# Optimization experiments

Hardware: AMD Instinct MI355X
Metric: run time of the kernel (lower is better)

The kernel has to match this reference:

```python
import jax, jax.numpy as jnp
import numpy as np

B = 8          # graphs (FOVs)
NPG = 16384    # clusters per graph
N = B * NPG
K = 6          # knn k=5+1, loop=True
E = N * K
C0PG = 2048    # superclusters_0 per graph
C0 = B * C0PG
C1PG = 256     # superclusters_1 per graph
C1 = B * C1PG
L = 10         # 4 cluster-level + 3 SC0 + 3 SC1 PointTransformerConv layers
D = 64


def setup_inputs() -> dict:
    key = jax.random.key(0)
    ks = jax.random.split(key, 20)
    s = 0.05  # weight scale for stable attention logits
    x = jax.random.normal(ks[0], (N, D), jnp.float32)
    pos_c = jax.random.uniform(ks[1], (N, 2), jnp.float32)
    dst_c = jnp.repeat(jnp.arange(N, dtype=jnp.int32), K)
    src_c = jax.random.randint(ks[2], (E,), 0, N, jnp.int32)
    src_c = src_c.at[::K].set(jnp.arange(N, dtype=jnp.int32))  # self-loops
    batch = (jnp.arange(N, dtype=jnp.int32) // NPG)
    sc_id0 = (jnp.arange(N, dtype=jnp.int32) % C0PG)   # every SC0 id present per graph
    pos_sc0 = jax.random.uniform(ks[3], (C0, 2), jnp.float32)
    sc_id1 = (jnp.arange(C0, dtype=jnp.int32) % C1PG)
    pos_sc1 = jax.random.uniform(ks[4], (C1, 2), jnp.float32)
    return dict(
        x=x, pos_c=pos_c, src_c=src_c, dst_c=dst_c, batch=batch,
        sc_id0=sc_id0, pos_sc0=pos_sc0, sc_id1=sc_id1, pos_sc1=pos_sc1,
        Wlin=jax.random.normal(ks[5], (L, D, D)) * s,
        Wsrc=jax.random.normal(ks[6], (L, D, D)) * s,
        Wdst=jax.random.normal(ks[7], (L, D, D)) * s,
        pW1=jax.random.normal(ks[8], (L, 2, D)) * s,
        pB1=jnp.zeros((L, D), jnp.float32),
        pW2=jax.random.normal(ks[9], (L, D, D)) * s,
        pB2=jnp.zeros((L, D), jnp.float32),
        aW1=jax.random.normal(ks[10], (L, D, D)) * s,
        aB1=jnp.zeros((L, D), jnp.float32),
        aW2=jax.random.normal(ks[11], (L, D, D)) * s,
        aB2=jnp.zeros((L, D), jnp.float32),
        head_w=jax.random.normal(ks[12], (D, 2)) * s,
        head_b=jnp.zeros((2,), jnp.float32),
    )


def mlp2(x, W1, b1, W2, b2):
    # PyG MLP(plain_last=False): Linear->ReLU twice (eval mode, BN at init = identity)
    h = jax.nn.relu(x @ W1 + b1)
    return jax.nn.relu(h @ W2 + b2)


def ptconv(h, pos, src, dst, n, p, l):
    # PointTransformerConv: delta = pos_nn(pos_i - pos_j);
    # alpha = softmax_i(attn_nn(lin_dst(x)_i - lin_src(x)_j + delta));
    # out_i = max_j alpha * (lin(x)_j + delta)
    xv = h @ p['Wlin'][l]
    a_src = h @ p['Wsrc'][l]
    a_dst = h @ p['Wdst'][l]
    delta = mlp2(pos[dst] - pos[src], p['pW1'][l], p['pB1'][l], p['pW2'][l], p['pB2'][l])
    a = mlp2(a_dst[dst] - a_src[src] + delta, p['aW1'][l], p['aB1'][l], p['aW2'][l], p['aB2'][l])
    m = jax.ops.segment_max(a, dst, num_segments=n)
    e = jnp.exp(a - m[dst])
    ssum = jax.ops.segment_sum(e, dst, num_segments=n)
    alpha = e / ssum[dst]
    return jax.ops.segment_max(alpha * (xv[src] + delta), dst, num_segments=n)


def gen_cluster(ids, batch, nb):
    mx = jax.ops.segment_max(ids, batch, num_segments=nb)
    off = jnp.cumsum(jnp.concatenate([jnp.zeros((1,), ids.dtype), mx + 1]))
    return ids + off[batch].astype(ids.dtype)


def knn_edges(pos, b, npg, k):
    # knn_graph(k, loop=True) per graph: src=neighbor, dst=center
    p = pos.reshape(b, npg, 2)
    sq = jnp.sum(p * p, axis=-1)
    d2 = sq[:, :, None] + sq[:, None, :] - 2.0 * jnp.einsum('bnd,bmd->bnm', p, p)
    idx = jax.lax.top_k(-d2, k)[1]  # [b, npg, k], includes self (d=0)
    src = (idx + (jnp.arange(b) * npg)[:, None, None]).reshape(-1).astype(jnp.int32)
    dst = jnp.repeat(jnp.arange(b * npg, dtype=jnp.int32), k)
    return src, dst


def reference(x, pos_c, src_c, dst_c, batch, sc_id0, pos_sc0, sc_id1, pos_sc1,
              Wlin, Wsrc, Wdst, pW1, pB1, pW2, pB2, aW1, aB1, aW2, aB2,
              head_w, head_b):
    p = dict(Wlin=Wlin, Wsrc=Wsrc, Wdst=Wdst, pW1=pW1, pB1=pB1, pW2=pW2, pB2=pB2,
             aW1=aW1, aB1=aB1, aW2=aW2, aB2=aB2)
    h = x
    for l in range(4):  # cluster_encoder_0..3 on clusters graph
        h = ptconv(h, pos_c, src_c, dst_c, N, p, l)
    # pool clusters -> superclusters_0
    cl0 = gen_cluster(sc_id0, batch, B)
    h0 = jax.ops.segment_max(h, cl0, num_segments=C0)
    batch0 = jax.ops.segment_max(batch, cl0, num_segments=C0)
    src0, dst0 = knn_edges(pos_sc0, B, C0PG, K)
    for l in range(4, 7):
        h0 = ptconv(h0, pos_sc0, src0, dst0, C0, p, l)
    # pool SC0 -> superclusters_1
    cl1 = gen_cluster(sc_id1, batch0, B)
    h1 = jax.ops.segment_max(h0, cl1, num_segments=C1)
    batch1 = jax.ops.segment_max(batch0, cl1, num_segments=C1)
    src1, dst1 = knn_edges(pos_sc1, B, C1PG, K)
    for l in range(7, 10):
        h1 = ptconv(h1, pos_sc1, src1, dst1, C1, p, l)
    g = jax.ops.segment_max(h1, batch1, num_segments=B)  # global_max_pool
    return g @ head_w + head_b
```

## Files before the change

kernel.cpp:

```cpp
#include <hip/hip_runtime.h>
#include <cstdint>

namespace {
constexpr int BG   = 8;
constexpr int NPG  = 16384;
constexpr int NN   = BG * NPG;
constexpr int KK   = 6;
constexpr int C0PG = 2048;
constexpr int C0N  = BG * C0PG;
constexpr int C1PG = 256;
constexpr int C1N  = BG * C1PG;
constexpr int D    = 64;
constexpr int SEG0 = C0PG / 256;
constexpr int VS   = 198;
constexpr int NMS  = 132;
}

__device__ __forceinline__ unsigned f2u_ord(float v) {
  unsigned u = __float_as_uint(v);
  return (u & 0x80000000u) ? ~u : (u | 0x80000000u);
}

__global__ void k_init_u32(unsigned* __restrict__ p, unsigned v, int n) {
  int i = blockIdx.x * blockDim.x + threadIdx.x;
  if (i < n) p[i] = v;
}

__global__ void k_seg_max_i32(const int* __restrict__ vals, const int* __restrict__ seg,
                              int* __restrict__ out, int n) {
  int i = blockIdx.x * blockDim.x + threadIdx.x;
  if (i < n) atomicMax(&out[seg[i]], vals[i]);
}

template <int NB>
__global__ __launch_bounds__(256) void k_seg_max_small(
    const int* __restrict__ vals, const int* __restrict__ seg,
    int* __restrict__ out, int n) {
  __shared__ int lmx[NB];
  int t = threadIdx.x;
  if (t < NB) lmx[t] = (int)0x80000000;
  __syncthreads();
  for (int i = blockIdx.x * 256 + t; i < n; i += gridDim.x * 256)
    atomicMax(&lmx[seg[i]], vals[i]);
  __syncthreads();
  if (t < NB) atomicMax(&out[t], lmx[t]);
}

__global__ void k_cumsum_off(const int* __restrict__ mx, int* __restrict__ off, int nb) {
  if (threadIdx.x == 0 && blockIdx.x == 0) {
    int a = 0; off[0] = 0;
    for (int b = 0; b < nb; ++b) { a += mx[b] + 1; off[b + 1] = a; }
  }
}

__global__ void k_gen_cl(const int* __restrict__ ids, const int* __restrict__ bt,
                         const int* __restrict__ off, int* __restrict__ cl, int n) {
  int i = blockIdx.x * blockDim.x + threadIdx.x;
  if (i < n) cl[i] = ids[i] + off[bt[i]];
}

__global__ void k_pool_f32(const float* __restrict__ h, const int* __restrict__ cl,
                           unsigned* __restrict__ outu, int total) {
  int i = blockIdx.x * blockDim.x + threadIdx.x;
  if (i < total) atomicMax(&outu[(size_t)cl[i >> 6] * D + (i & 63)], f2u_ord(h[i]));
}

__global__ void k_decode_f32(unsigned* __restrict__ p, int n) {
  int i = blockIdx.x * blockDim.x + threadIdx.x;
  if (i < n) { unsigned u = p[i]; p[i] = (u & 0x80000000u) ? (u ^ 0x80000000u) : ~u; }
}

__global__ __launch_bounds__(256) void k_knn(const float* __restrict__ pos, int npg,
                                             int* __restrict__ srcOut) {
  #pragma clang fp contract(off)
  __shared__ float px[2048], py[2048], sq[2048];
  int t = threadIdx.x;
  int nglob = blockIdx.x * 256 + t;
  int graph = nglob / npg;
  int base = graph * npg;
  for (int i = t; i < npg; i += 256) {
    float xx = pos[2 * (base + i)];
    float yy = pos[2 * (base + i) + 1];
    px[i] = xx; py[i] = yy;
    float a = xx * xx; float b = yy * yy;
    sq[i] = a + b;
  }
  __syncthreads();
  int i = nglob - base;
  float xi = px[i], yi = py[i], sqi = sq[i];
  float bd[KK]; int bi[KK];
  #pragma unroll
  for (int q = 0; q < KK; ++q) { bd[q] = 3.4e38f; bi[q] = 0; }
  for (int j = 0; j < npg; ++j) {
    float t1 = xi * px[j];
    float t2 = yi * py[j];
    float dot = t1 + t2;
    float d2 = (sqi + sq[j]) - 2.0f * dot;
    if (d2 < bd[KK - 1]) {
      bd[KK - 1] = d2; bi[KK - 1] = j;
      #pragma unroll
      for (int q = KK - 1; q > 0; --q) {
        if (bd[q] < bd[q - 1]) {
          float td = bd[q]; bd[q] = bd[q - 1]; bd[q - 1] = td;
          int ti = bi[q]; bi[q] = bi[q - 1]; bi[q - 1] = ti;
        }
      }
    }
  }
  #pragma unroll
  for (int q = 0; q < KK; ++q) srcOut[(size_t)nglob * KK + q] = base + bi[q];
}

__global__ __launch_bounds__(256) void k_knn_part(const float* __restrict__ pos, int npg,
                                                  int nseg,
                                                  float* __restrict__ outD,
                                                  int* __restrict__ outI) {
  #pragma clang fp contract(off)
  __shared__ float cx[256], cy[256], cs[256];
  int t = threadIdx.x;
  int qt = blockIdx.x / nseg;
  int s  = blockIdx.x % nseg;
  int qlo = qt * 256;
  int graph = qlo / npg;
  int base = graph * npg;
  int cbase = base + s * 256;
  {
    float xx = pos[2 * (cbase + t)];
    float yy = pos[2 * (cbase + t) + 1];
    cx[t] = xx; cy[t] = yy;
    float a = xx * xx; float b = yy * yy;
    cs[t] = a + b;
  }
  __syncthreads();
  int q = qlo + t;
  float xi = pos[2 * q], yi = pos[2 * q + 1];
  float qa = xi * xi; float qb = yi * yi;
  float sqi = qa + qb;
  float bd[KK]; int bi[KK];
  #pragma unroll
  for (int u = 0; u < KK; ++u) { bd[u] = 3.4e38f; bi[u] = 0; }
  for (int j = 0; j < 256; ++j) {
    float t1 = xi * cx[j];
    float t2 = yi * cy[j];
    float dot = t1 + t2;
    float d2 = (sqi + cs[j]) - 2.0f * dot;
    if (d2 < bd[KK - 1]) {
      bd[KK - 1] = d2; bi[KK - 1] = cbase + j;
      #pragma unroll
      for (int u = KK - 1; u > 0; --u) {
        if (bd[u] < bd[u - 1]) {
          float td = bd[u]; bd[u] = bd[u - 1]; bd[u - 1] = td;
          int ti = bi[u]; bi[u] = bi[u - 1]; bi[u - 1] = ti;
        }
      }
    }
  }
  size_t ob = (size_t)q * (nseg * KK) + (size_t)s * KK;
  #pragma unroll
  for (int u = 0; u < KK; ++u) { outD[ob + u] = bd[u]; outI[ob + u] = bi[u]; }
}

__global__ void k_knn_merge(const float* __restrict__ inD, const int* __restrict__ inI,
                            int nseg, int* __restrict__ srcOut, int nq) {
  int q = blockIdx.x * blockDim.x + threadIdx.x;
  if (q >= nq) return;
  float bd[KK]; int bi[KK];
  #pragma unroll
  for (int u = 0; u < KK; ++u) { bd[u] = 3.4e38f; bi[u] = 0x7fffffff; }
  size_t ib = (size_t)q * (nseg * KK);
  for (int e = 0; e < nseg * KK; ++e) {
    float d = inD[ib + e]; int ix = inI[ib + e];
    bool lt = (d < bd[KK - 1]) || (d == bd[KK - 1] && ix < bi[KK - 1]);
    if (lt) {
      bd[KK - 1] = d; bi[KK - 1] = ix;
      #pragma unroll
      for (int u = KK - 1; u > 0; --u) {
        bool sw = (bd[u] < bd[u - 1]) || (bd[u] == bd[u - 1] && bi[u] < bi[u - 1]);
        if (sw) {
          float td = bd[u]; bd[u] = bd[u - 1]; bd[u - 1] = td;
          int ti = bi[u]; bi[u] = bi[u - 1]; bi[u - 1] = ti;
        }
      }
    }
  }
  #pragma unroll
  for (int u = 0; u < KK; ++u) srcOut[(size_t)q * KK + u] = bi[u];
}

__global__ void __launch_bounds__(256)
__attribute__((amdgpu_waves_per_eu(4, 4)))
k_node_mm(const float* __restrict__ hin,
    const float* __restrict__ Wl, const float* __restrict__ Ws, const float* __restrict__ Wd,
    float* __restrict__ xv, float* __restrict__ as_, float* __restrict__ ad_) {
  __shared__ float wbuf[2048];
  __shared__ float vbuf[32 * NMS];
  int t = threadIdx.x;
  size_t nb = (size_t)blockIdx.x * 128;
  int ng = t >> 3, cb = t & 7, c0 = cb * 8;
  const float* Wm[3] = {Wl, Ws, Wd};
  float* Om[3] = {xv, as_, ad_};
  const float4* h4 = (const float4*)hin;
  float4 wreg0 = ((const float4*)Wl)[t];
  float4 wreg1 = ((const float4*)Wl)[256 + t];
  float acc[3][32];
  #pragma unroll
  for (int m = 0; m < 3; ++m)
    #pragma unroll
    for (int i = 0; i < 32; ++i) acc[m][i] = 0.0f;
  #pragma unroll
  for (int kh = 0; kh < 2; ++kh) {
    #pragma unroll
    for (int r = 0; r < 4; ++r) {
      int flat = r * 256 + t;
      int n = flat >> 3, kq = flat & 7;
      float4 hv = h4[(nb + n) * 16 + kh * 8 + kq];
      vbuf[(kq * 4 + 0) * NMS + n] = hv.x;
      vbuf[(kq * 4 + 1) * NMS + n] = hv.y;
      vbuf[(kq * 4 + 2) * NMS + n] = hv.z;
      vbuf[(kq * 4 + 3) * NMS + n] = hv.w;
    }
    #pragma unroll
    for (int m = 0; m < 3; ++m) {
      {
        float4* wb = (float4*)wbuf;
        wb[t] = wreg0;
        wb[256 + t] = wreg1;
      }
      if (!(kh == 1 && m == 2)) {
        const float* nW = (m < 2) ? Wm[m + 1] : Wm[0];
        int nkh = (m < 2) ? kh : kh + 1;
        const float4* nxt = (const float4*)nW + nkh * 512;
        wreg0 = nxt[t];
        wreg1 = nxt[256 + t];
      }
      __syncthreads();
      #pragma clang loop unroll_count(2)
      for (int kk = 0; kk < 32; ++kk) {
        float4 v4 = *(const float4*)&vbuf[kk * NMS + 4 * ng];
        float4 w0 = *(const float4*)&wbuf[kk * 64 + c0];
        float4 w1 = *(const float4*)&wbuf[kk * 64 + c0 + 4];
        float vv[4] = {v4.x, v4.y, v4.z, v4.w};
        float wv[8] = {w0.x, w0.y, w0.z, w0.w, w1.x, w1.y, w1.z, w1.w};
        #pragma unroll
        for (int ni = 0; ni < 4; ++ni)
          #pragma unroll
          for (int c = 0; c < 8; ++c)
            acc[m][ni * 8 + c] = fmaf(vv[ni], wv[c], acc[m][ni * 8 + c]);
      }
      __syncthreads();
    }
  }
  #pragma unroll
  for (int m = 0; m < 3; ++m) {
    float* O = Om[m];
    #pragma unroll
    for (int ni = 0; ni < 4; ++ni) {
      *(float4*)(O + (nb + 4 * ng + ni) * 64 + c0) =
          make_float4(acc[m][ni * 8 + 0], acc[m][ni * 8 + 1],
                      acc[m][ni * 8 + 2], acc[m][ni * 8 + 3]);
      *(float4*)(O + (nb + 4 * ng + ni) * 64 + c0 + 4) =
          make_float4(acc[m][ni * 8 + 4], acc[m][ni * 8 + 5],
                      acc[m][ni * 8 + 6], acc[m][ni * 8 + 7]);
    }
  }
}

__global__ void __launch_bounds__(256)
__attribute__((amdgpu_waves_per_eu(4, 4)))
k_edge_fused(
    const float* __restrict__ pos, const int* __restrict__ srcA,
    const float* __restrict__ as_, const float* __restrict__ ad_,
    const float* __restrict__ xv,
    const float* __restrict__ pW1, const float* __restrict__ pB1,
    const float* __restrict__ pW2, const float* __restrict__ pB2,
    const float* __restrict__ aW1, const float* __restrict__ aB1,
    const float* __restrict__ aW2, const float* __restrict__ aB2,
    float* __restrict__ hout) {
  __shared__ float wbuf[2048];
  __shared__ float vbuf[32 * VS];
  __shared__ float sbuf[192];
  __shared__ float pdxs[192], pdys[192];
  __shared__ int   srcb[192];
  int t = threadIdx.x;
  int nb = blockIdx.x * 32;
  int ng = t >> 3;
  int cb = t & 7;
  int cl = 4 * cb;
  int ch = 32 + 4 * cb;
  int node = nb + ng;

  float4 wreg0 = ((const float4*)pW2)[t];
  float4 wreg1 = ((const float4*)pW2)[256 + t];
  if (t < 192) {
    int s = srcA[(size_t)nb * KK + t];
    srcb[t] = s;
    int dn = nb + t / KK;
    float2 pd = *(const float2*)(pos + 2 * (size_t)dn);
    float2 ps = *(const float2*)(pos + 2 * (size_t)s);
    pdxs[t] = pd.x - ps.x;
    pdys[t] = pd.y - ps.y;
    sbuf[t] = (t < 128) ? pW1[t] : pB1[t - 128];
  }
  __syncthreads();

  float d[48];
  {
    float4 b0 = *(const float4*)(pB2 + cl);
    float4 b1 = *(const float4*)(pB2 + ch);
    #pragma unroll
    for (int j = 0; j < 6; ++j) {
      d[j * 8 + 0] = b0.x; d[j * 8 + 1] = b0.y; d[j * 8 + 2] = b0.z; d[j * 8 + 3] = b0.w;
      d[j * 8 + 4] = b1.x; d[j * 8 + 5] = b1.y; d[j * 8 + 6] = b1.z; d[j * 8 + 7] = b1.w;
    }
  }
  #pragma unroll
  for (int h = 0; h < 2; ++h) {
    {
      float4* wb = (float4*)wbuf;
      wb[t] = wreg0;
      wb[256 + t] = wreg1;
    }
    {
      const float4* nxt = (h == 0) ? ((const float4*)pW2 + 512) : ((const float4*)aW1);
      wreg0 = nxt[t];
      wreg1 = nxt[256 + t];
    }
    if (t < 192) {
      float px = pdxs[t], py = pdys[t];
      #pragma clang loop unroll_count(4)
      for (int kk = 0; kk < 32; ++kk) {
        int k = h * 32 + kk;
        float p0 = px * sbuf[k];
        float p1 = py * sbuf[64 + k];
        float ph = fmaxf((p0 + p1) + sbuf[128 + k], 0.0f);
        vbuf[kk * VS + t] = ph;
      }
    }
    __syncthreads();
    #pragma clang loop unroll_count(2)
    for (int kk = 0; kk < 32; ++kk) {
      float2 v01 = *(const float2*)&vbuf[kk * VS + 6 * ng];
      float2 v23 = *(const float2*)&vbuf[kk * VS + 6 * ng + 2];
      float2 v45 = *(const float2*)&vbuf[kk * VS + 6 * ng + 4];
      float4 w0 = *(const float4*)&wbuf[kk * 64 + cl];
      float4 w1 = *(const float4*)&wbuf[kk * 64 + ch];
      float vv[6] = {v01.x, v01.y, v23.x, v23.y, v45.x, v45.y};
      float wv[8] = {w0.x, w0.y, w0.z, w0.w, w1.x, w1.y, w1.z, w1.w};
      #pragma unroll
      for (int j = 0; j < 6; ++j)
        #pragma unroll
        for (int c = 0; c < 8; ++c)
          d[j * 8 + c] = fmaf(vv[j], wv[c], d[j * 8 + c]);
    }
    __syncthreads();
  }
  #pragma unroll
  for (int i = 0; i < 48; ++i) d[i] = fmaxf(d[i], 0.0f);

  float r[48];
  {
    float4 b0 = *(const float4*)(aB1 + cl);
    float4 b1 = *(const float4*)(aB1 + ch);
    #pragma unroll
    for (int j = 0; j < 6; ++j) {
      r[j * 8 + 0] = b0.x; r[j * 8 + 1] = b0.y; r[j * 8 + 2] = b0.z; r[j * 8 + 3] = b0.w;
      r[j * 8 + 4] = b1.x; r[j * 8 + 5] = b1.y; r[j * 8 + 6] = b1.z; r[j * 8 + 7] = b1.w;
    }
  }
  #pragma unroll
  for (int h = 0; h < 2; ++h) {
    {
      float4* wb = (float4*)wbuf;
      wb[t] = wreg0;
      wb[256 + t] = wreg1;
    }
    {
      const float4* nxt = (h == 0) ? ((const float4*)aW1 + 512) : ((const float4*)aW2);
      wreg0 = nxt[t];
      wreg1 = nxt[256 + t];
    }
    {
      int cbase = h ? ch : cl;
      float4 av = *(const float4*)(ad_ + (size_t)node * 64 + cbase);
      float vtmp[6][4];
      #pragma unroll
      for (int j = 0; j < 6; ++j) {
        int s = srcb[6 * ng + j];
        float4 sv = *(const float4*)(as_ + (size_t)s * 64 + cbase);
        vtmp[j][0] = (av.x - sv.x) + d[j * 8 + 4 * h + 0];
        vtmp[j][1] = (av.y - sv.y) + d[j * 8 + 4 * h + 1];
        vtmp[j][2] = (av.z - sv.z) + d[j * 8 + 4 * h + 2];
        vtmp[j][3] = (av.w - sv.w) + d[j * 8 + 4 * h + 3];
      }
      #pragma unroll
      for (int cj = 0; cj < 4; ++cj)
        #pragma unroll
        for (int jp = 0; jp < 3; ++jp)
          *(float2*)&vbuf[(4 * cb + cj) * VS + 6 * ng + 2 * jp] =
              make_float2(vtmp[2 * jp][cj], vtmp[2 * jp + 1][cj]);
    }
    __syncthreads();
    #pragma clang loop unroll_count(2)
    for (int kk = 0; kk < 32; ++kk) {
      float2 v01 = *(const float2*)&vbuf[kk * VS + 6 * ng];
      float2 v23 = *(const float2*)&vbuf[kk * VS + 6 * ng + 2];
      float2 v45 = *(const float2*)&vbuf[kk * VS + 6 * ng + 4];
      float4 w0 = *(const float4*)&wbuf[kk * 64 + cl];
      float4 w1 = *(const float4*)&wbuf[kk * 64 + ch];
      float vv[6] = {v01.x, v01.y, v23.x, v23.y, v45.x, v45.y};
      float wv[8] = {w0.x, w0.y, w0.z, w0.w, w1.x, w1.y, w1.z, w1.w};
      #pragma unroll
      for (int j = 0; j < 6; ++j)
        #pragma unroll
        for (int c = 0; c < 8; ++c)
          r[j * 8 + c] = fmaf(vv[j], wv[c], r[j * 8 + c]);
    }
    __syncthreads();
  }
  #pragma unroll
  for (int i = 0; i < 48; ++i) r[i] = fmaxf(r[i], 0.0f);

  float a[48];
  {
    float4 b0 = *(const float4*)(aB2 + cl);
    float4 b1 = *(const float4*)(aB2 + ch);
    #pragma unroll
    for (int j = 0; j < 6; ++j) {
      a[j * 8 + 0] = b0.x; a[j * 8 + 1] = b0.y; a[j * 8 + 2] = b0.z; a[j * 8 + 3] = b0.w;
      a[j * 8 + 4] = b1.x; a[j * 8 + 5] = b1.y; a[j * 8 + 6] = b1.z; a[j * 8 + 7] = b1.w;
    }
  }
  #pragma unroll
  for (int h = 0; h < 2; ++h) {
    {
      float4* wb = (float4*)wbuf;
      wb[t] = wreg0;
      wb[256 + t] = wreg1;
    }
    if (h == 0) {
      const float4* nxt = (const float4*)aW2 + 512;
      wreg0 = nxt[t];
      wreg1 = nxt[256 + t];
    }
    #pragma unroll
    for (int cj = 0; cj < 4; ++cj)
      #pragma unroll
      for (int jp = 0; jp < 3; ++jp)
        *(float2*)&vbuf[(4 * cb + cj) * VS + 6 * ng + 2 * jp] =
            make_float2(r[(2 * jp) * 8 + 4 * h + cj], r[(2 * jp + 1) * 8 + 4 * h + cj]);
    __syncthreads();
    #pragma clang loop unroll_count(2)
    for (int kk = 0; kk < 32; ++kk) {
      float2 v01 = *(const float2*)&vbuf[kk * VS + 6 * ng];
      float2 v23 = *(const float2*)&vbuf[kk * VS + 6 * ng + 2];
      float2 v45 = *(const float2*)&vbuf[kk * VS + 6 * ng + 4];
      float4 w0 = *(const float4*)&wbuf[kk * 64 + cl];
      float4 w1 = *(const float4*)&wbuf[kk * 64 + ch];
      float vv[6] = {v01.x, v01.y, v23.x, v23.y, v45.x, v45.y};
      float wv[8] = {w0.x, w0.y, w0.z, w0.w, w1.x, w1.y, w1.z, w1.w};
      #pragma unroll
      for (int j = 0; j < 6; ++j)
        #pragma unroll
        for (int c = 0; c < 8; ++c)
          a[j * 8 + c] = fmaf(vv[j], wv[c], a[j * 8 + c]);
    }
    __syncthreads();
  }
  #pragma unroll
  for (int i = 0; i < 48; ++i) a[i] = fmaxf(a[i], 0.0f);

  float m8[8], ss[8], out[8];
  #pragma unroll
  for (int c = 0; c < 8; ++c) m8[c] = a[c];
  #pragma unroll
  for (int j = 1; j < 6; ++j)
    #pragma unroll
    for (int c = 0; c < 8; ++c) m8[c] = fmaxf(m8[c], a[j * 8 + c]);
  #pragma unroll
  for (int c = 0; c < 8; ++c) ss[c] = 0.0f;
  #pragma unroll
  for (int j = 0; j < 6; ++j)
    #pragma unroll
    for (int c = 0; c < 8; ++c) ss[c] += expf(a[j * 8 + c] - m8[c]);
  #pragma unroll
  for (int j = 0; j < 6; ++j) {
    int s = srcb[6 * ng + j];
    float4 x0 = *(const float4*)(xv + (size_t)s * 64 + cl);
    float4 x1 = *(const float4*)(xv + (size_t)s * 64 + ch);
    float xa[8] = {x0.x, x0.y, x0.z, x0.w, x1.x, x1.y, x1.z, x1.w};
    #pragma unroll
    for (int c = 0; c < 8; ++c) {
      float ej = expf(a[j * 8 + c] - m8[c]);
      float alpha = ej / ss[c];
      float val = alpha * (xa[c] + d[j * 8 + c]);
      out[c] = (j == 0) ? val : fmaxf(out[c], val);
    }
  }
  *(float4*)(hout + (size_t)node * 64 + cl) = make_float4(out[0], out[1], out[2], out[3]);
  *(float4*)(hout + (size_t)node * 64 + ch) = make_float4(out[4], out[5], out[6], out[7]);
}

__global__ void k_head(const float* __restrict__ g, const float* __restrict__ hw,
                       const float* __restrict__ hb, float* __restrict__ out) {
  int t = threadIdx.x;
  if (t >= BG * 2) return;
  int b = t >> 1, o = t & 1;
  float acc = 0.0f;
  for (int k = 0; k < D; ++k) acc = fmaf(g[b * D + k], hw[k * 2 + o], acc);
  out[b * 2 + o] = acc + hb[o];
}

extern "C" void kernel_launch(void* const* d_in, const int* in_sizes, int n_in,
                              void* d_out, int out_size, void* d_ws, size_t ws_size,
                              hipStream_t stream) {
  (void)in_sizes; (void)n_in; (void)out_size; (void)ws_size;
  const float* x      = (const float*)d_in[0];
  const float* pos_c  = (const float*)d_in[1];
  const int*   src_c  = (const int*)d_in[2];
  const int*   batch  = (const int*)d_in[4];
  const int*   sc_id0 = (const int*)d_in[5];
  const float* pos_s0 = (const float*)d_in[6];
  const int*   sc_id1 = (const int*)d_in[7];
  const float* pos_s1 = (const float*)d_in[8];
  const float* Wlin = (const float*)d_in[9];
  const float* Wsrc = (const float*)d_in[10];
  const float* Wdst = (const float*)d_in[11];
  const float* pW1  = (const float*)d_in[12];
  const float* pB1  = (const float*)d_in[13];
  const float* pW2  = (const float*)d_in[14];
  const float* pB2  = (const float*)d_in[15];
  const float* aW1  = (const float*)d_in[16];
  const float* aB1  = (const float*)d_in[17];
  const float* aW2  = (const float*)d_in[18];
  const float* aB2  = (const float*)d_in[19];
  const float* hw   = (const float*)d_in[20];
  const float* hb   = (const float*)d_in[21];
  float* outp = (float*)d_out;

  char* ws = (char*)d_ws;
  size_t off = 0;
  auto alloc = [&](size_t bytes) -> void* {
    void* p = ws + off; off = (off + bytes + 255) & ~(size_t)255; return p;
  };
  float* h   = (float*)alloc((size_t)NN * D * 4);
  float* xv  = (float*)alloc((size_t)NN * D * 4);
  float* as_ = (float*)alloc((size_t)NN * D * 4);
  float* ad_ = (float*)alloc((size_t)NN * D * 4);
  float* h0  = (float*)alloc((size_t)C0N * D * 4);
  float* h1  = (float*)alloc((size_t)C1N * D * 4);
  float* g   = (float*)alloc((size_t)BG * D * 4);
  int* cl0   = (int*)alloc((size_t)NN * 4);
  int* cl1   = (int*)alloc((size_t)C0N * 4);
  int* b0    = (int*)alloc((size_t)C0N * 4);
  int* b1    = (int*)alloc((size_t)C1N * 4);
  int* src0  = (int*)alloc((size_t)C0N * KK * 4);
  int* src1  = (int*)alloc((size_t)C1N * KK * 4);
  float* kd  = (float*)alloc((size_t)C0N * SEG0 * KK * 4);
  int*   ki  = (int*)alloc((size_t)C0N * SEG0 * KK * 4);
  int* mx    = (int*)alloc(256);
  int* offb  = (int*)alloc(256);

  auto ptconv = [&](int n, const float* pos, const int* srcA,
                    const float* hin, float* hout, int l) {
    k_node_mm<<<n / 128, 256, 0, stream>>>(hin,
        Wlin + (size_t)l * 4096, Wsrc + (size_t)l * 4096, Wdst + (size_t)l * 4096,
        xv, as_, ad_);
    k_edge_fused<<<n / 32, 256, 0, stream>>>(pos, srcA, as_, ad_, xv,
        pW1 + (size_t)l * 128, pB1 + (size_t)l * 64,
        pW2 + (size_t)l * 4096, pB2 + (size_t)l * 64,
        aW1 + (size_t)l * 4096, aB1 + (size_t)l * 64,
        aW2 + (size_t)l * 4096, aB2 + (size_t)l * 64,
        hout);
  };

  k_init_u32<<<1, 64, 0, stream>>>((unsigned*)mx, 0x80000000u, BG);
  k_seg_max_small<BG><<<64, 256, 0, stream>>>(sc_id0, batch, mx, NN);
  k_cumsum_off<<<1, 1, 0, stream>>>(mx, offb, BG);
  k_gen_cl<<<NN / 256, 256, 0, stream>>>(sc_id0, batch, offb, cl0, NN);
  k_init_u32<<<(C0N + 255) / 256, 256, 0, stream>>>((unsigned*)b0, 0x80000000u, C0N);
  k_seg_max_i32<<<NN / 256, 256, 0, stream>>>(batch, cl0, b0, NN);
  k_knn_part<<<(C0N / 256) * SEG0, 256, 0, stream>>>(pos_s0, C0PG, SEG0, kd, ki);
  k_knn_merge<<<C0N / 256, 256, 0, stream>>>(kd, ki, SEG0, src0, C0N);
  k_init_u32<<<1, 64, 0, stream>>>((unsigned*)mx, 0x80000000u, BG);
  k_seg_max_small<BG><<<64, 256, 0, stream>>>(sc_id1, b0, mx, C0N);
  k_cumsum_off<<<1, 1, 0, stream>>>(mx, offb, BG);
  k_gen_cl<<<C0N / 256, 256, 0, stream>>>(sc_id1, b0, offb, cl1, C0N);
  k_init_u32<<<(C1N + 255) / 256, 256, 0, stream>>>((unsigned*)b1, 0x80000000u, C1N);
  k_seg_max_i32<<<C0N / 256, 256, 0, stream>>>(b0, cl1, b1, C0N);
  k_knn<<<C1N / 256, 256, 0, stream>>>(pos_s1, C1PG, src1);

  ptconv(NN, pos_c, src_c, x, h, 0);
  for (int l = 1; l < 4; ++l) ptconv(NN, pos_c, src_c, h, h, l);
  k_init_u32<<<C0N * D / 256, 256, 0, stream>>>((unsigned*)h0, 0x007fffffu, C0N * D);
  k_pool_f32<<<NN * D / 256, 256, 0, stream>>>(h, cl0, (unsigned*)h0, NN * D);
  k_decode_f32<<<C0N * D / 256, 256, 0, stream>>>((unsigned*)h0, C0N * D);
  for (int l = 4; l < 7; ++l) ptconv(C0N, pos_s0, src0, h0, h0, l);
  k_init_u32<<<C1N * D / 256, 256, 0, stream>>>((unsigned*)h1, 0x007fffffu, C1N * D);
  k_pool_f32<<<C0N * D / 256, 256, 0, stream>>>(h0, cl1, (unsigned*)h1, C0N * D);
  k_decode_f32<<<C1N * D / 256, 256, 0, stream>>>((unsigned*)h1, C1N * D);
  for (int l = 7; l < 10; ++l) ptconv(C1N, pos_s1, src1, h1, h1, l);
  k_init_u32<<<(BG * D + 255) / 256, 256, 0, stream>>>((unsigned*)g, 0x007fffffu, BG * D);
  k_pool_f32<<<C1N * D / 256, 256, 0, stream>>>(h1, b1, (unsigned*)g, C1N * D);
  k_decode_f32<<<(BG * D + 255) / 256, 256, 0, stream>>>((unsigned*)g, BG * D);
  k_head<<<1, 64, 0, stream>>>(g, hw, hb, outp);
}
```

Measured before the change: 1.934 ms.

## Pad edge smem rows to 8 columns, relax edge occupancy, drop node weight prefetch

The edge kernel's shared activation buffer now gives each node 8 columns for its 6 edges (row stride 260). Each thread reads its edge values with two float4 loads instead of three float2 loads, and writes them with a float4 plus a float2. The edge kernel's occupancy hint drops from 4 to 3 waves per EU, which gives it more registers. The node matmul kernel no longer prefetches the next weight tile through registers; it loads weights straight into shared memory and its kh loop is no longer force-unrolled, which lowers register pressure but exposes global load latency.

```diff
diff --git a/kernel.cpp b/kernel.cpp
--- a/kernel.cpp
+++ b/kernel.cpp
@@ -12,7 +12,7 @@
 constexpr int C1N  = BG * C1PG;
 constexpr int D    = 64;
 constexpr int SEG0 = C0PG / 256;
-constexpr int VS   = 198;
+constexpr int VS8  = 260;
 constexpr int NMS  = 132;
 }
 
@@ -200,14 +200,11 @@
   const float* Wm[3] = {Wl, Ws, Wd};
   float* Om[3] = {xv, as_, ad_};
   const float4* h4 = (const float4*)hin;
-  float4 wreg0 = ((const float4*)Wl)[t];
-  float4 wreg1 = ((const float4*)Wl)[256 + t];
   float acc[3][32];
   #pragma unroll
   for (int m = 0; m < 3; ++m)
     #pragma unroll
     for (int i = 0; i < 32; ++i) acc[m][i] = 0.0f;
-  #pragma unroll
   for (int kh = 0; kh < 2; ++kh) {
     #pragma unroll
     for (int r = 0; r < 4; ++r) {
@@ -222,16 +219,10 @@
     #pragma unroll
     for (int m = 0; m < 3; ++m) {
       {
+        const float4* w4 = (const float4*)Wm[m] + kh * 512;
         float4* wb = (float4*)wbuf;
-        wb[t] = wreg0;
-        wb[256 + t] = wreg1;
-      }
-      if (!(kh == 1 && m == 2)) {
-        const float* nW = (m < 2) ? Wm[m + 1] : Wm[0];
-        int nkh = (m < 2) ? kh : kh + 1;
-        const float4* nxt = (const float4*)nW + nkh * 512;
-        wreg0 = nxt[t];
-        wreg1 = nxt[256 + t];
+        wb[t] = w4[t];
+        wb[256 + t] = w4[256 + t];
       }
       __syncthreads();
       #pragma clang loop unroll_count(2)
@@ -266,7 +257,7 @@
 }
 
 __global__ void __launch_bounds__(256)
-__attribute__((amdgpu_waves_per_eu(4, 4)))
+__attribute__((amdgpu_waves_per_eu(3, 3)))
 k_edge_fused(
     const float* __restrict__ pos, const int* __restrict__ srcA,
     const float* __restrict__ as_, const float* __restrict__ ad_,
@@ -277,7 +268,7 @@
     const float* __restrict__ aW2, const float* __restrict__ aB2,
     float* __restrict__ hout) {
   __shared__ float wbuf[2048];
-  __shared__ float vbuf[32 * VS];
+  __shared__ float vbuf[32 * VS8];
   __shared__ float sbuf[192];
   __shared__ float pdxs[192], pdys[192];
   __shared__ int   srcb[192];
@@ -288,9 +279,11 @@
   int cl = 4 * cb;
   int ch = 32 + 4 * cb;
   int node = nb + ng;
+  int ecol = 8 * ng;
 
   float4 wreg0 = ((const float4*)pW2)[t];
   float4 wreg1 = ((const float4*)pW2)[256 + t];
+  int mycol = 8 * (t / 6) + (t % 6);
   if (t < 192) {
     int s = srcA[(size_t)nb * KK + t];
     srcb[t] = s;
@@ -333,18 +326,17 @@
         float p0 = px * sbuf[k];
         float p1 = py * sbuf[64 + k];
         float ph = fmaxf((p0 + p1) + sbuf[128 + k], 0.0f);
-        vbuf[kk * VS + t] = ph;
+        vbuf[kk * VS8 + mycol] = ph;
       }
     }
     __syncthreads();
     #pragma clang loop unroll_count(2)
     for (int kk = 0; kk < 32; ++kk) {
-      float2 v01 = *(const float2*)&vbuf[kk * VS + 6 * ng];
-      float2 v23 = *(const float2*)&vbuf[kk * VS + 6 * ng + 2];
-      float2 v45 = *(const float2*)&vbuf[kk * VS + 6 * ng + 4];
+      float4 va = *(const float4*)&vbuf[kk * VS8 + ecol];
+      float4 vb = *(const float4*)&vbuf[kk * VS8 + ecol + 4];
       float4 w0 = *(const float4*)&wbuf[kk * 64 + cl];
       float4 w1 = *(const float4*)&wbuf[kk * 64 + ch];
-      float vv[6] = {v01.x, v01.y, v23.x, v23.y, v45.x, v45.y};
+      float vv[6] = {va.x, va.y, va.z, va.w, vb.x, vb.y};
       float wv[8] = {w0.x, w0.y, w0.z, w0.w, w1.x, w1.y, w1.z, w1.w};
       #pragma unroll
       for (int j = 0; j < 6; ++j)
@@ -393,21 +385,21 @@
         vtmp[j][3] = (av.w - sv.w) + d[j * 8 + 4 * h + 3];
       }
       #pragma unroll
-      for (int cj = 0; cj < 4; ++cj)
-        #pragma unroll
-        for (int jp = 0; jp < 3; ++jp)
-          *(float2*)&vbuf[(4 * cb + cj) * VS + 6 * ng + 2 * jp] =
-              make_float2(vtmp[2 * jp][cj], vtmp[2 * jp + 1][cj]);
+      for (int cj = 0; cj < 4; ++cj) {
+        int rr = 4 * cb + cj;
+        *(float4*)&vbuf[rr * VS8 + ecol] =
+            make_float4(vtmp[0][cj], vtmp[1][cj], vtmp[2][cj], vtmp[3][cj]);
+        *(float2*)&vbuf[rr * VS8 + ecol + 4] = make_float2(vtmp[4][cj], vtmp[5][cj]);
+      }
     }
     __syncthreads();
     #pragma clang loop unroll_count(2)
     for (int kk = 0; kk < 32; ++kk) {
-      float2 v01 = *(const float2*)&vbuf[kk * VS + 6 * ng];
-      float2 v23 = *(const float2*)&vbuf[kk * VS + 6 * ng + 2];
-      float2 v45 = *(const float2*)&vbuf[kk * VS + 6 * ng + 4];
+      float4 va = *(const float4*)&vbuf[kk * VS8 + ecol];
+      float4 vb = *(const float4*)&vbuf[kk * VS8 + ecol + 4];
       float4 w0 = *(const float4*)&wbuf[kk * 64 + cl];
       float4 w1 = *(const float4*)&wbuf[kk * 64 + ch];
-      float vv[6] = {v01.x, v01.y, v23.x, v23.y, v45.x, v45.y};
+      float vv[6] = {va.x, va.y, va.z, va.w, vb.x, vb.y};
       float wv[8] = {w0.x, w0.y, w0.z, w0.w, w1.x, w1.y, w1.z, w1.w};
       #pragma unroll
       for (int j = 0; j < 6; ++j)
@@ -443,20 +435,22 @@
       wreg1 = nxt[256 + t];
     }
     #pragma unroll
-    for (int cj = 0; cj < 4; ++cj)
-      #pragma unroll
-      for (int jp = 0; jp < 3; ++jp)
-        *(float2*)&vbuf[(4 * cb + cj) * VS + 6 * ng + 2 * jp] =
-            make_float2(r[(2 * jp) * 8 + 4 * h + cj], r[(2 * jp + 1) * 8 + 4 * h + cj]);
+    for (int cj = 0; cj < 4; ++cj) {
+      int rr = 4 * cb + cj;
+      *(float4*)&vbuf[rr * VS8 + ecol] =
+          make_float4(r[0 * 8 + 4 * h + cj], r[1 * 8 + 4 * h + cj],
+                      r[2 * 8 + 4 * h + cj], r[3 * 8 + 4 * h + cj]);
+      *(float2*)&vbuf[rr * VS8 + ecol + 4] =
+          make_float2(r[4 * 8 + 4 * h + cj], r[5 * 8 + 4 * h + cj]);
+    }
     __syncthreads();
     #pragma clang loop unroll_count(2)
     for (int kk = 0; kk < 32; ++kk) {
-      float2 v01 = *(const float2*)&vbuf[kk * VS + 6 * ng];
-      float2 v23 = *(const float2*)&vbuf[kk * VS + 6 * ng + 2];
-      float2 v45 = *(const float2*)&vbuf[kk * VS + 6 * ng + 4];
+      float4 va = *(const float4*)&vbuf[kk * VS8 + ecol];
+      float4 vb = *(const float4*)&vbuf[kk * VS8 + ecol + 4];
       float4 w0 = *(const float4*)&wbuf[kk * 64 + cl];
       float4 w1 = *(const float4*)&wbuf[kk * 64 + ch];
-      float vv[6] = {v01.x, v01.y, v23.x, v23.y, v45.x, v45.y};
+      float vv[6] = {va.x, va.y, va.z, va.w, vb.x, vb.y};
       float wv[8] = {w0.x, w0.y, w0.z, w0.w, w1.x, w1.y, w1.z, w1.w};
       #pragma unroll
       for (int j = 0; j < 6; ++j)
```

Result: faster. 1.874 ms (-3.1%).
